# Optimization experiments

Hardware: AMD Instinct MI355X
Metric: run time of the kernel (lower is better)

## Reference

```python
import jax, jax.numpy as jnp
import numpy as np

# Map flattened lm index (l<=3, 16 components) -> l value, used to expand
# the per-l tp_weights [E,4,C] to per-lm weights [E,16,C].
L_OF_LM = jnp.array([0, 1, 1, 1, 2, 2, 2, 2, 2, 3, 3, 3, 3, 3, 3, 3], dtype=jnp.int32)

NNODES = 25000
NEDGES = 400000
NCHAN = 64


def setup_inputs() -> dict:
    key = jax.random.key(0)
    k1, k2, k3, k4 = jax.random.split(key, 4)
    node_feats = jax.random.normal(k1, (NNODES, NCHAN), dtype=jnp.float32)
    edge_attrs = jax.random.normal(k2, (NEDGES, 16), dtype=jnp.float32)
    tp_weights = jax.random.normal(k3, (NEDGES, 4, NCHAN), dtype=jnp.float32)
    receiver_list = jnp.sort(
        jax.random.randint(k4, (NEDGES,), 0, NNODES, dtype=jnp.int64)
    )
    return {
        "node_feats": node_feats,
        "edge_attrs": edge_attrs,
        "tp_weights": tp_weights,
        "receiver_list": receiver_list,
        "nnodes": NNODES,
    }


def reference(node_feats, edge_attrs, tp_weights, receiver_list, nnodes):
    # Gather per-edge node features: [E, C]
    feats = node_feats[receiver_list]
    # Expand per-l weights to per-lm weights: [E, 16, C]
    w_lm = tp_weights[:, L_OF_LM, :]
    # Invariant tensor product message: [E, 16, C]
    msg = edge_attrs[:, :, None] * w_lm * feats[:, None, :]
    # Scatter-add messages to receiver nodes: [nnodes, 16, C]
    return jax.ops.segment_sum(msg, receiver_list, num_segments=nnodes)
```

## Files before the change

kernel.cpp:

```cpp
#include <hip/hip_runtime.h>


#define FMA16(EA_OFF, W0, W1, W2, W3)                                         \
    acc[0]  += ea[EA_OFF + 0]  * W0;                                          \
    acc[1]  += ea[EA_OFF + 1]  * W1;                                          \
    acc[2]  += ea[EA_OFF + 2]  * W1;                                          \
    acc[3]  += ea[EA_OFF + 3]  * W1;                                          \
    acc[4]  += ea[EA_OFF + 4]  * W2;                                          \
    acc[5]  += ea[EA_OFF + 5]  * W2;                                          \
    acc[6]  += ea[EA_OFF + 6]  * W2;                                          \
    acc[7]  += ea[EA_OFF + 7]  * W2;                                          \
    acc[8]  += ea[EA_OFF + 8]  * W2;                                          \
    acc[9]  += ea[EA_OFF + 9]  * W3;                                          \
    acc[10] += ea[EA_OFF + 10] * W3;                                          \
    acc[11] += ea[EA_OFF + 11] * W3;                                          \
    acc[12] += ea[EA_OFF + 12] * W3;                                          \
    acc[13] += ea[EA_OFF + 13] * W3;                                          \
    acc[14] += ea[EA_OFF + 14] * W3;                                          \
    acc[15] += ea[EA_OFF + 15] * W3;

#define LOAD_W8(DST, EBASE)                                                   \
    {                                                                         \
        const float* wp = tp_weights + (size_t)(EBASE) * 256 + lane;          \
        DST[0] = __builtin_nontemporal_load(wp);                              \
        DST[1] = __builtin_nontemporal_load(wp + 64);                         \
        DST[2] = __builtin_nontemporal_load(wp + 128);                        \
        DST[3] = __builtin_nontemporal_load(wp + 192);                        \
        DST[4] = __builtin_nontemporal_load(wp + 256);                        \
        DST[5] = __builtin_nontemporal_load(wp + 320);                        \
        DST[6] = __builtin_nontemporal_load(wp + 384);                        \
        DST[7] = __builtin_nontemporal_load(wp + 448);                        \
    }

#define EA_FMA(EBASE, W)                                                      \
    {                                                                         \
        const float* eap = edge_attrs + (size_t)(EBASE) * 16;                 \
        float ea[32];                                                         \
        _Pragma("unroll")                                                     \
        for (int i = 0; i < 32; ++i) ea[i] = eap[i];                          \
        FMA16(0,  W[0], W[1], W[2], W[3])                                     \
        FMA16(16, W[4], W[5], W[6], W[7])                                     \
    }

__global__ __launch_bounds__(256) void bounds_kernel(
    const int* __restrict__ recv, int nedges, int nnodes,
    int* __restrict__ off)
{
    const int n = blockIdx.x * blockDim.x + threadIdx.x;
    if (n > nnodes) return;
    int lo = 0, hi = nedges;
    while (lo < hi) { int mid = (lo + hi) >> 1; if (recv[mid] < n) lo = mid + 1; else hi = mid; }
    off[n] = lo;
}

__global__ __launch_bounds__(256, 8) void imp_tp_main(
    const float* __restrict__ node_feats,
    const float* __restrict__ edge_attrs,
    const float* __restrict__ tp_weights,
    const int*   __restrict__ off,
    int nnodes,
    float* __restrict__ out)
{
    const int wave = (blockIdx.x * blockDim.x + threadIdx.x) >> 6;
    const int lane = threadIdx.x & 63;
    if (wave >= nnodes) return;
    const int n = wave;

    const int start = __builtin_amdgcn_readfirstlane(off[n]);
    const int end   = __builtin_amdgcn_readfirstlane(off[n + 1]);

    const float nf = node_feats[(size_t)n * 64 + lane];

    float acc[16];
    #pragma unroll
    for (int i = 0; i < 16; ++i) acc[i] = 0.f;

    const int npairs = (end - start) >> 1;
    int e = start;
    float wa[8], wb[8];

    if (npairs > 0) LOAD_W8(wa, e)
    if (npairs > 1) LOAD_W8(wb, e + 2)

    int p = 0;
    for (; p + 3 < npairs; p += 2, e += 4) {
        EA_FMA(e, wa)
        LOAD_W8(wa, e + 4)
        EA_FMA(e + 2, wb)
        LOAD_W8(wb, e + 6)
    }
    const int r = npairs - p;
    if (r == 3) {
        EA_FMA(e, wa)
        LOAD_W8(wa, e + 4)
        EA_FMA(e + 2, wb)
        EA_FMA(e + 4, wa)
        e += 6;
    } else if (r == 2) {
        EA_FMA(e, wa)
        EA_FMA(e + 2, wb)
        e += 4;
    } else if (r == 1) {
        EA_FMA(e, wa)
        e += 2;
    }
    if (e < end) {
        const float* wp = tp_weights + (size_t)e * 256 + lane;
        const float a0 = __builtin_nontemporal_load(wp);
        const float a1 = __builtin_nontemporal_load(wp + 64);
        const float a2 = __builtin_nontemporal_load(wp + 128);
        const float a3 = __builtin_nontemporal_load(wp + 192);
        const float* eap = edge_attrs + (size_t)e * 16;
        float ea[16];
        #pragma unroll
        for (int i = 0; i < 16; ++i) ea[i] = eap[i];
        FMA16(0, a0, a1, a2, a3)
    }

    float* o = out + (size_t)n * 1024 + lane;
    #pragma unroll
    for (int lm = 0; lm < 16; ++lm)
        __builtin_nontemporal_store(acc[lm] * nf, o + lm * 64);
}

__global__ __launch_bounds__(256) void imp_tp_fallback(
    const float* __restrict__ node_feats,
    const float* __restrict__ edge_attrs,
    const float* __restrict__ tp_weights,
    const int*   __restrict__ recv,
    int nnodes, int nedges,
    float* __restrict__ out)
{
    const int wave = (blockIdx.x * blockDim.x + threadIdx.x) >> 6;
    const int lane = threadIdx.x & 63;
    if (wave >= nnodes) return;
    const int n = wave;

    int lo = 0, hi = nedges;
    while (lo < hi) { int mid = (lo + hi) >> 1; if (recv[mid] < n) lo = mid + 1; else hi = mid; }
    const int start = lo;
    hi = nedges;
    while (lo < hi) { int mid = (lo + hi) >> 1; if (recv[mid] < n + 1) lo = mid + 1; else hi = mid; }
    const int end = lo;

    float acc[16];
    #pragma unroll
    for (int i = 0; i < 16; ++i) acc[i] = 0.f;

    for (int e = start; e < end; ++e) {
        const float4* ea4 = reinterpret_cast<const float4*>(edge_attrs + (size_t)e * 16);
        const float4 ea0 = ea4[0];
        const float4 ea1 = ea4[1];
        const float4 ea2 = ea4[2];
        const float4 ea3 = ea4[3];
        const float* w = tp_weights + (size_t)e * 256 + lane;
        const float w0 = w[0];
        const float w1 = w[64];
        const float w2 = w[128];
        const float w3 = w[192];

        acc[0]  += ea0.x * w0;
        acc[1]  += ea0.y * w1;
        acc[2]  += ea0.z * w1;
        acc[3]  += ea0.w * w1;
        acc[4]  += ea1.x * w2;
        acc[5]  += ea1.y * w2;
        acc[6]  += ea1.z * w2;
        acc[7]  += ea1.w * w2;
        acc[8]  += ea2.x * w2;
        acc[9]  += ea2.y * w3;
        acc[10] += ea2.z * w3;
        acc[11] += ea2.w * w3;
        acc[12] += ea3.x * w3;
        acc[13] += ea3.y * w3;
        acc[14] += ea3.z * w3;
        acc[15] += ea3.w * w3;
    }

    const float nf = node_feats[(size_t)n * 64 + lane];
    float* o = out + (size_t)n * 1024 + lane;
    #pragma unroll
    for (int lm = 0; lm < 16; ++lm) o[lm * 64] = acc[lm] * nf;
}

extern "C" void kernel_launch(void* const* d_in, const int* in_sizes, int n_in,
                              void* d_out, int out_size, void* d_ws, size_t ws_size,
                              hipStream_t stream) {
    const float* node_feats = (const float*)d_in[0];
    const float* edge_attrs = (const float*)d_in[1];
    const float* tp_weights = (const float*)d_in[2];
    const int*   recv       = (const int*)d_in[3];
    float* out = (float*)d_out;

    const int nnodes = in_sizes[0] / 64;
    const int nedges = in_sizes[1] / 16;

    const int threads = 256;
    const int blocks = (nnodes * 64 + threads - 1) / threads;

    if (ws_size >= (size_t)(nnodes + 1) * sizeof(int)) {
        int* off = (int*)d_ws;
        const int bthreads = 256;
        const int bblocks = (nnodes + 1 + bthreads - 1) / bthreads;
        bounds_kernel<<<bblocks, bthreads, 0, stream>>>(recv, nedges, nnodes, off);
        imp_tp_main<<<blocks, threads, 0, stream>>>(
            node_feats, edge_attrs, tp_weights, off, nnodes, out);
    } else {
        imp_tp_fallback<<<blocks, threads, 0, stream>>>(
            node_feats, edge_attrs, tp_weights, recv, nnodes, nedges, out);
    }
}
```

Baseline: 103.1 us.

## Prefetch edge attributes alongside weights and build offsets by per-edge scatter

```diff
diff --git a/kernel.cpp b/kernel.cpp
--- a/kernel.cpp
+++ b/kernel.cpp
@@ -1,23 +1,27 @@
 #include <hip/hip_runtime.h>
 
 
-#define FMA16(EA_OFF, W0, W1, W2, W3)                                         \
-    acc[0]  += ea[EA_OFF + 0]  * W0;                                          \
-    acc[1]  += ea[EA_OFF + 1]  * W1;                                          \
-    acc[2]  += ea[EA_OFF + 2]  * W1;                                          \
-    acc[3]  += ea[EA_OFF + 3]  * W1;                                          \
-    acc[4]  += ea[EA_OFF + 4]  * W2;                                          \
-    acc[5]  += ea[EA_OFF + 5]  * W2;                                          \
-    acc[6]  += ea[EA_OFF + 6]  * W2;                                          \
-    acc[7]  += ea[EA_OFF + 7]  * W2;                                          \
-    acc[8]  += ea[EA_OFF + 8]  * W2;                                          \
-    acc[9]  += ea[EA_OFF + 9]  * W3;                                          \
-    acc[10] += ea[EA_OFF + 10] * W3;                                          \
-    acc[11] += ea[EA_OFF + 11] * W3;                                          \
-    acc[12] += ea[EA_OFF + 12] * W3;                                          \
-    acc[13] += ea[EA_OFF + 13] * W3;                                          \
-    acc[14] += ea[EA_OFF + 14] * W3;                                          \
-    acc[15] += ea[EA_OFF + 15] * W3;
+#define FMA16A(EA, OFF, W0, W1, W2, W3)                                       \
+    acc[0]  += EA[OFF + 0]  * W0;                                             \
+    acc[1]  += EA[OFF + 1]  * W1;                                             \
+    acc[2]  += EA[OFF + 2]  * W1;                                             \
+    acc[3]  += EA[OFF + 3]  * W1;                                             \
+    acc[4]  += EA[OFF + 4]  * W2;                                             \
+    acc[5]  += EA[OFF + 5]  * W2;                                             \
+    acc[6]  += EA[OFF + 6]  * W2;                                             \
+    acc[7]  += EA[OFF + 7]  * W2;                                             \
+    acc[8]  += EA[OFF + 8]  * W2;                                             \
+    acc[9]  += EA[OFF + 9]  * W3;                                             \
+    acc[10] += EA[OFF + 10] * W3;                                             \
+    acc[11] += EA[OFF + 11] * W3;                                             \
+    acc[12] += EA[OFF + 12] * W3;                                             \
+    acc[13] += EA[OFF + 13] * W3;                                             \
+    acc[14] += EA[OFF + 14] * W3;                                             \
+    acc[15] += EA[OFF + 15] * W3;
+
+#define FMA32(EA, W)                                                          \
+    FMA16A(EA, 0,  W[0], W[1], W[2], W[3])                                    \
+    FMA16A(EA, 16, W[4], W[5], W[6], W[7])
 
 #define LOAD_W8(DST, EBASE)                                                   \
     {                                                                         \
@@ -32,25 +36,24 @@
         DST[7] = __builtin_nontemporal_load(wp + 448);                        \
     }
 
-#define EA_FMA(EBASE, W)                                                      \
+#define LOAD_EA(DST, EBASE)                                                   \
     {                                                                         \
         const float* eap = edge_attrs + (size_t)(EBASE) * 16;                 \
-        float ea[32];                                                         \
         _Pragma("unroll")                                                     \
-        for (int i = 0; i < 32; ++i) ea[i] = eap[i];                          \
-        FMA16(0,  W[0], W[1], W[2], W[3])                                     \
-        FMA16(16, W[4], W[5], W[6], W[7])                                     \
-    }
-
-__global__ __launch_bounds__(256) void bounds_kernel(
+        for (int i = 0; i < 32; ++i) DST[i] = eap[i];                         \
+    }
+
+__global__ __launch_bounds__(256) void bounds_scatter(
     const int* __restrict__ recv, int nedges, int nnodes,
     int* __restrict__ off)
 {
-    const int n = blockIdx.x * blockDim.x + threadIdx.x;
-    if (n > nnodes) return;
-    int lo = 0, hi = nedges;
-    while (lo < hi) { int mid = (lo + hi) >> 1; if (recv[mid] < n) lo = mid + 1; else hi = mid; }
-    off[n] = lo;
+    const int e = blockIdx.x * blockDim.x + threadIdx.x;
+    if (e >= nedges) return;
+    const int r  = recv[e];
+    const int rn = (e + 1 < nedges) ? recv[e + 1] : nnodes;
+    if (e == 0)
+        for (int n = 0; n <= r; ++n) off[n] = 0;
+    for (int n = r + 1; n <= rn; ++n) off[n] = e + 1;
 }
 
 __global__ __launch_bounds__(256, 8) void imp_tp_main(
@@ -78,30 +81,31 @@
     const int npairs = (end - start) >> 1;
     int e = start;
     float wa[8], wb[8];
-
-    if (npairs > 0) LOAD_W8(wa, e)
-    if (npairs > 1) LOAD_W8(wb, e + 2)
+    float eaA[32], eaB[32];
+
+    if (npairs > 0) { LOAD_W8(wa, e)     LOAD_EA(eaA, e) }
+    if (npairs > 1) { LOAD_W8(wb, e + 2) LOAD_EA(eaB, e + 2) }
 
     int p = 0;
     for (; p + 3 < npairs; p += 2, e += 4) {
-        EA_FMA(e, wa)
-        LOAD_W8(wa, e + 4)
-        EA_FMA(e + 2, wb)
-        LOAD_W8(wb, e + 6)
+        FMA32(eaA, wa)
+        LOAD_W8(wa, e + 4) LOAD_EA(eaA, e + 4)
+        FMA32(eaB, wb)
+        LOAD_W8(wb, e + 6) LOAD_EA(eaB, e + 6)
     }
     const int r = npairs - p;
     if (r == 3) {
-        EA_FMA(e, wa)
-        LOAD_W8(wa, e + 4)
-        EA_FMA(e + 2, wb)
-        EA_FMA(e + 4, wa)
+        FMA32(eaA, wa)
+        LOAD_W8(wa, e + 4) LOAD_EA(eaA, e + 4)
+        FMA32(eaB, wb)
+        FMA32(eaA, wa)
         e += 6;
     } else if (r == 2) {
-        EA_FMA(e, wa)
-        EA_FMA(e + 2, wb)
+        FMA32(eaA, wa)
+        FMA32(eaB, wb)
         e += 4;
     } else if (r == 1) {
-        EA_FMA(e, wa)
+        FMA32(eaA, wa)
         e += 2;
     }
     if (e < end) {
@@ -110,11 +114,11 @@
         const float a1 = __builtin_nontemporal_load(wp + 64);
         const float a2 = __builtin_nontemporal_load(wp + 128);
         const float a3 = __builtin_nontemporal_load(wp + 192);
+        float ea[16];
         const float* eap = edge_attrs + (size_t)e * 16;
-        float ea[16];
         #pragma unroll
         for (int i = 0; i < 16; ++i) ea[i] = eap[i];
-        FMA16(0, a0, a1, a2, a3)
+        FMA16A(ea, 0, a0, a1, a2, a3)
     }
 
     float* o = out + (size_t)n * 1024 + lane;
@@ -201,8 +205,8 @@
     if (ws_size >= (size_t)(nnodes + 1) * sizeof(int)) {
         int* off = (int*)d_ws;
         const int bthreads = 256;
-        const int bblocks = (nnodes + 1 + bthreads - 1) / bthreads;
-        bounds_kernel<<<bblocks, bthreads, 0, stream>>>(recv, nedges, nnodes, off);
+        const int bblocks = (nedges + bthreads - 1) / bthreads;
+        bounds_scatter<<<bblocks, bthreads, 0, stream>>>(recv, nedges, nnodes, off);
         imp_tp_main<<<blocks, threads, 0, stream>>>(
             node_feats, edge_attrs, tp_weights, off, nnodes, out);
     } else {
```

Measured after the change: 104.8 us. Within noise of the previous version (+1.6%).
